# Performance work log

Hardware: AMD Instinct MI355X
Metric: run time of the kernel (lower is better)

The kernel has to match this reference:

```python
import jax, jax.numpy as jnp
import numpy as np

DIM_IN = 1024
DIM_OUT = 1024
NUM_HEADS = 16
HEAD_DIM = DIM_OUT // NUM_HEADS


def setup_inputs() -> dict:
    key = jax.random.key(0)
    ks = jax.random.split(key, 7)
    s = 1.0 / np.sqrt(DIM_IN)
    x = jax.random.normal(ks[0], (4, 2048, DIM_IN), dtype=jnp.float32)
    Wq = jax.random.uniform(ks[1], (DIM_IN, DIM_OUT), jnp.float32, -s, s)
    bq = jax.random.uniform(ks[2], (DIM_OUT,), jnp.float32, -s, s)
    Wk = jax.random.uniform(ks[3], (DIM_IN, DIM_OUT), jnp.float32, -s, s)
    bk = jax.random.uniform(ks[4], (DIM_OUT,), jnp.float32, -s, s)
    Wv = jax.random.uniform(ks[5], (DIM_IN, DIM_OUT), jnp.float32, -s, s)
    bv = jax.random.uniform(ks[6], (DIM_OUT,), jnp.float32, -s, s)
    return {"x": x, "Wq": Wq, "bq": bq, "Wk": Wk, "bk": bk, "Wv": Wv, "bv": bv}


def reference(x, Wq, bq, Wk, bk, Wv, bv):
    B, S, _ = x.shape
    scale = HEAD_DIM ** 0.5
    # project and split heads: [B, H, S, Dh]
    def heads(W, b):
        return (x @ W + b).reshape(B, S, NUM_HEADS, HEAD_DIM).transpose(0, 2, 1, 3)
    q = heads(Wq, bq)
    k = heads(Wk, bk)
    v = heads(Wv, bv)
    scores = jnp.einsum("bhqd,bhkd->bhqk", q, k) / scale  # [B,H,S,S]
    attn = jax.nn.softmax(scores, axis=-1)
    out = jnp.einsum("bhqk,bhkd->bhqd", attn, v)
    return out.transpose(0, 2, 1, 3).reshape(B, S, DIM_OUT)
```

## Files before the change

kernel.cpp:

```cpp
#include <hip/hip_runtime.h>
#include <hip/hip_bf16.h>


#define DIM  1024
#define SEQ  2048
#define BATCH 4
#define NH   16
#define HD   64

typedef __bf16 bf16x8 __attribute__((ext_vector_type(8)));
typedef short  s16x4  __attribute__((ext_vector_type(4)));
typedef float  f32x4  __attribute__((ext_vector_type(4)));
typedef unsigned int uint4v __attribute__((ext_vector_type(4)));

static __device__ __forceinline__ f32x4 mfma16(s16x4 a, s16x4 b, f32x4 c) {
    return __builtin_amdgcn_mfma_f32_16x16x16bf16_1k(a, b, c, 0, 0, 0);
}

static __device__ __forceinline__ unsigned short f2b(float f) {
    __bf16 h = (__bf16)f;
    return __builtin_bit_cast(unsigned short, h);
}

static __device__ __forceinline__ void load_lds16(const unsigned short* g,
                                                  unsigned short* l) {
    __builtin_amdgcn_global_load_lds(
        (const __attribute__((address_space(1))) void*)g,
        (__attribute__((address_space(3))) void*)l, 16, 0, 0);
}

__global__ __launch_bounds__(256) void cvt_x_k(const float* __restrict__ x,
                                               unsigned short* __restrict__ xb) {
    size_t i = ((size_t)blockIdx.x * 256 + threadIdx.x) * 8;
    const f32x4* s = (const f32x4*)(x + i);
    f32x4 a0 = s[0], a1 = s[1];
    bf16x8 v;
    for (int j = 0; j < 4; j++) { v[j] = (__bf16)a0[j]; v[4 + j] = (__bf16)a1[j]; }
    *(bf16x8*)(xb + i) = v;
}

__global__ void transpose_w_k(const float* __restrict__ Wq,
                              const float* __restrict__ Wk,
                              const float* __restrict__ Wv,
                              unsigned short* __restrict__ Wt) {
    __shared__ unsigned short t[32][33];
    int z = blockIdx.z;
    const float* W = (z == 0) ? Wq : (z == 1) ? Wk : Wv;
    unsigned short* o = Wt + (size_t)z * DIM * DIM;
    int tx = threadIdx.x;
    int n0 = blockIdx.x * 32, k0 = blockIdx.y * 32;
    for (int j = threadIdx.y; j < 32; j += 8)
        t[j][tx] = f2b(W[(size_t)(k0 + j) * DIM + n0 + tx]);
    __syncthreads();
    for (int j = threadIdx.y; j < 32; j += 8)
        o[(size_t)(n0 + j) * DIM + k0 + tx] = t[tx][j];
}

__global__ __launch_bounds__(512) void qkv_gemm_k(
    const unsigned short* __restrict__ xb,
    const unsigned short* __restrict__ WtBase,
    const float* __restrict__ bq,
    const float* __restrict__ bk,
    const float* __restrict__ bv,
    unsigned short* __restrict__ Qo,
    unsigned short* __restrict__ Ko,
    unsigned short* __restrict__ Vto) {
    __shared__ __align__(16) unsigned short As[256 * 64];
    __shared__ __align__(16) unsigned short Bs[128 * 64];
    int tid = threadIdx.x, wave = tid >> 6, lane = tid & 63;
    int quad = lane >> 4, lc = lane & 15;
    int m0 = blockIdx.y * 256, n0 = blockIdx.x * 128;
    int z = blockIdx.z;
    const unsigned short* Wt = WtBase + (size_t)z * DIM * DIM;
    int wm = (wave >> 1) * 64, wn = (wave & 1) * 64;
    int swzlo = lc & 7;

    f32x4 acc[4][4] = {};

    for (int k0 = 0; k0 < DIM; k0 += 64) {
        __syncthreads();
        #pragma unroll
        for (int p = 0; p < 4; p++) {
            int c = tid + p * 512, r = c >> 3, cc = (c & 7) ^ (r & 7);
            load_lds16(xb + (size_t)(m0 + r) * DIM + k0 + cc * 8, &As[c * 8]);
        }
        #pragma unroll
        for (int p = 0; p < 2; p++) {
            int c = tid + p * 512, r = c >> 3, cc = (c & 7) ^ (r & 7);
            load_lds16(Wt + (size_t)(n0 + r) * DIM + k0 + cc * 8, &Bs[c * 8]);
        }
        __syncthreads();
        #pragma unroll
        for (int kk = 0; kk < 2; kk++) {
            int off = ((kk * 4 + quad) ^ swzlo) * 8;
            bf16x8 af[4], bfr[4];
            for (int mt = 0; mt < 4; mt++)
                af[mt] = *(const bf16x8*)&As[(wm + mt * 16 + lc) * 64 + off];
            for (int nt = 0; nt < 4; nt++)
                bfr[nt] = *(const bf16x8*)&Bs[(wn + nt * 16 + lc) * 64 + off];
            for (int mt = 0; mt < 4; mt++)
                for (int nt = 0; nt < 4; nt++)
                    acc[mt][nt] = __builtin_amdgcn_mfma_f32_16x16x32_bf16(
                        af[mt], bfr[nt], acc[mt][nt], 0, 0, 0);
        }
    }

    const float* bias = (z == 0) ? bq : (z == 1) ? bk : bv;
    float scale = (z == 0) ? 0.18033688011112042f : 1.0f;

    if (z != 2) {
        for (int nt = 0; nt < 4; nt++) {
            int n = n0 + wn + nt * 16 + lc;
            float bvl = bias[n];
            int h = n >> 6, d = n & 63;
            for (int mt = 0; mt < 4; mt++) {
                for (int r = 0; r < 4; r++) {
                    int m = m0 + wm + mt * 16 + quad * 4 + r;
                    int b = m >> 11, s = m & 2047;
                    unsigned short ub = f2b((acc[mt][nt][r] + bvl) * scale);
                    if (z == 0)
                        Qo[((size_t)(b * NH + h) * SEQ + s) * HD + d] = ub;
                    else
                        Ko[((size_t)(b * NH + h) * SEQ + s) * HD + d] = ub;
                }
            }
        }
    } else {
        __syncthreads();
        unsigned short* T = As + wave * 1024;
        int h = (n0 + wn) >> 6;
        int d = lane;
        for (int mt = 0; mt < 4; mt++) {
            for (int nt = 0; nt < 4; nt++) {
                int n = n0 + wn + nt * 16 + lc;
                float bvl = bias[n];
                s16x4 v4;
                for (int r = 0; r < 4; r++)
                    v4[r] = (short)f2b(acc[mt][nt][r] + bvl);
                *(s16x4*)&T[(nt * 16 + lc) * 16 + quad * 4] = v4;
            }
            int s_base = m0 + wm + mt * 16;
            int b = s_base >> 11, sl = s_base & 2047;
            unsigned short* dst =
                Vto + ((size_t)(b * NH + h) * HD + d) * SEQ + sl;
            uint4v t0 = *(const uint4v*)&T[d * 16];
            uint4v t1 = *(const uint4v*)&T[d * 16 + 8];
            *(uint4v*)&dst[0] = t0;
            *(uint4v*)&dst[8] = t1;
        }
    }
}

__global__ __launch_bounds__(256) void attn_k(
    const unsigned short* __restrict__ Q,
    const unsigned short* __restrict__ K,
    const unsigned short* __restrict__ Vt,
    float* __restrict__ out) {
    __shared__ __align__(16) unsigned short KV[2 * 8192];

    int tid = threadIdx.x, wave = tid >> 6, lane = tid & 63;
    int quad = lane >> 4, lc = lane & 15;
    int swz = lc & 7;
    int bid = blockIdx.x;
    int j = bid >> 3;
    int bh = (bid & 7) * 8 + (j >> 4);
    int qt = j & 15;
    int b = bh >> 4, h = bh & 15;
    const unsigned short* Qg = Q + ((size_t)bh * SEQ + qt * 128) * HD;
    const unsigned short* Kg = K + (size_t)bh * SEQ * HD;
    const unsigned short* Vg = Vt + (size_t)bh * HD * SEQ;

    bf16x8 qf0[2], qf1[2];
    {
        const unsigned short* q0 = Qg + (size_t)(wave * 32 + lc) * HD + quad * 8;
        const unsigned short* q1 = q0 + 16 * HD;
        qf0[0] = *(const bf16x8*)q0;  qf0[1] = *(const bf16x8*)(q0 + 32);
        qf1[0] = *(const bf16x8*)q1;  qf1[1] = *(const bf16x8*)(q1 + 32);
    }

    f32x4 o[4][2] = {};
    float rsum0 = 0.0f, rsum1 = 0.0f;

    {
        unsigned short* Ks = KV;
        unsigned short* Vs = KV + 4096;
        #pragma unroll
        for (int p = 0; p < 2; p++) {
            int c = tid + p * 256, r = c >> 3, cc = c & 7;
            int sc8 = (cc ^ (r & 7)) * 8;
            load_lds16(Kg + (size_t)r * HD + sc8, &Ks[c * 8]);
            load_lds16(Vg + (size_t)r * SEQ + sc8, &Vs[c * 8]);
        }
    }

    for (int t0 = 0; t0 < SEQ; t0 += 64) {
        int cur = (t0 >> 6) & 1;
        unsigned short* Ks = KV + cur * 8192;
        unsigned short* Vs = Ks + 4096;
        __syncthreads();

        if (t0 + 64 < SEQ) {
            unsigned short* Kn = KV + (cur ^ 1) * 8192;
            unsigned short* Vn = Kn + 4096;
            #pragma unroll
            for (int p = 0; p < 2; p++) {
                int c = tid + p * 256, r = c >> 3, cc = c & 7;
                int sc8 = (cc ^ (r & 7)) * 8;
                load_lds16(Kg + (size_t)(t0 + 64 + r) * HD + sc8, &Kn[c * 8]);
                load_lds16(Vg + (size_t)r * SEQ + (t0 + 64) + sc8, &Vn[c * 8]);
            }
        }

        s16x4 pf[4][2];
        __builtin_amdgcn_s_setprio(1);
        #pragma unroll
        for (int kt = 0; kt < 4; kt++) {
            f32x4 sA = {}, sB = {};
            #pragma unroll
            for (int ks = 0; ks < 2; ks++) {
                bf16x8 kf = *(const bf16x8*)
                    &Ks[(kt * 16 + lc) * 64 + ((ks * 4 + quad) ^ swz) * 8];
                sA = __builtin_amdgcn_mfma_f32_16x16x32_bf16(kf, qf0[ks], sA, 0, 0, 0);
                sB = __builtin_amdgcn_mfma_f32_16x16x32_bf16(kf, qf1[ks], sB, 0, 0, 0);
            }
            #pragma unroll
            for (int r = 0; r < 4; r++) {
                float pa = __builtin_amdgcn_exp2f(sA[r]);
                float pb = __builtin_amdgcn_exp2f(sB[r]);
                rsum0 += pa; rsum1 += pb;
                pf[kt][0][r] = (short)f2b(pa);
                pf[kt][1][r] = (short)f2b(pb);
            }
        }

        #pragma unroll
        for (int dt = 0; dt < 4; dt++) {
            #pragma unroll
            for (int kt = 0; kt < 4; kt++) {
                s16x4 vf = *(const s16x4*)
                    &Vs[(dt * 16 + lc) * 64 +
                        ((2 * kt + (quad >> 1)) ^ swz) * 8 + (quad & 1) * 4];
                o[dt][0] = mfma16(vf, pf[kt][0], o[dt][0]);
                o[dt][1] = mfma16(vf, pf[kt][1], o[dt][1]);
            }
        }
        __builtin_amdgcn_s_setprio(0);
    }

    rsum0 += __shfl_xor(rsum0, 16); rsum0 += __shfl_xor(rsum0, 32);
    rsum1 += __shfl_xor(rsum1, 16); rsum1 += __shfl_xor(rsum1, 32);
    float inv0 = 1.0f / rsum0, inv1 = 1.0f / rsum1;

    float* o0 = out + ((size_t)b * SEQ + qt * 128 + wave * 32 + lc) * DIM
                + h * HD + quad * 4;
    float* o1 = o0 + (size_t)16 * DIM;
    #pragma unroll
    for (int dt = 0; dt < 4; dt++) {
        f32x4 s0 = o[dt][0]; s0 *= inv0;
        f32x4 s1 = o[dt][1]; s1 *= inv1;
        *(f32x4*)&o0[dt * 16] = s0;
        *(f32x4*)&o1[dt * 16] = s1;
    }
}

extern "C" void kernel_launch(void* const* d_in, const int* in_sizes, int n_in,
                              void* d_out, int out_size, void* d_ws, size_t ws_size,
                              hipStream_t stream) {
    (void)in_sizes; (void)n_in; (void)out_size; (void)ws_size;
    const float* x  = (const float*)d_in[0];
    const float* Wq = (const float*)d_in[1];
    const float* bq = (const float*)d_in[2];
    const float* Wk = (const float*)d_in[3];
    const float* bk = (const float*)d_in[4];
    const float* Wv = (const float*)d_in[5];
    const float* bv = (const float*)d_in[6];

    char* ws = (char*)d_ws;
    unsigned short* Wt = (unsigned short*)ws;
    unsigned short* Qb = (unsigned short*)(ws + (size_t)6 * 1024 * 1024);
    unsigned short* Kb = Qb + (size_t)BATCH * NH * SEQ * HD;
    unsigned short* Vb = Kb + (size_t)BATCH * NH * SEQ * HD;
    unsigned short* xb = (unsigned short*)d_out;

    cvt_x_k<<<dim3(4096), dim3(256), 0, stream>>>(x, xb);
    transpose_w_k<<<dim3(32, 32, 3), dim3(32, 8), 0, stream>>>(Wq, Wk, Wv, Wt);
    qkv_gemm_k<<<dim3(8, 32, 3), dim3(512), 0, stream>>>(xb, Wt, bq, bk, bv, Qb, Kb, Vb);
    attn_k<<<dim3(1024), dim3(256), 0, stream>>>(Qb, Kb, Vb, (float*)d_out);
}
```

Baseline: 259.0 us.

## Vectorize QKV epilogue stores and pad V tile via register-staged loads

The QKV GEMM is split into separate Q/K and V paths. For Q/K the MFMA operands are swapped so each lane holds four consecutive output columns, allowing 8-byte vector stores and a vector bias load. For V it drops the LDS transpose and writes 4-element vectors directly into the transposed layout. In attention, V tiles are staged through registers into a padded LDS layout (stride 72) instead of an XOR swizzle, with the LDS write placed between the score and PV phases. The aim is fewer scalar global stores and cheaper V fragment addressing. The cost is more register pressure, and the V prefetch now writes LDS synchronously.

```diff
diff --git a/kernel.cpp b/kernel.cpp
--- a/kernel.cpp
+++ b/kernel.cpp
@@ -73,80 +73,96 @@
     int z = blockIdx.z;
     const unsigned short* Wt = WtBase + (size_t)z * DIM * DIM;
     int wm = (wave >> 1) * 64, wn = (wave & 1) * 64;
-    int swzlo = lc & 7;
+    int swzlo = lc & 15 & 7;
 
     f32x4 acc[4][4] = {};
 
-    for (int k0 = 0; k0 < DIM; k0 += 64) {
-        __syncthreads();
-        #pragma unroll
-        for (int p = 0; p < 4; p++) {
-            int c = tid + p * 512, r = c >> 3, cc = (c & 7) ^ (r & 7);
-            load_lds16(xb + (size_t)(m0 + r) * DIM + k0 + cc * 8, &As[c * 8]);
-        }
-        #pragma unroll
-        for (int p = 0; p < 2; p++) {
-            int c = tid + p * 512, r = c >> 3, cc = (c & 7) ^ (r & 7);
-            load_lds16(Wt + (size_t)(n0 + r) * DIM + k0 + cc * 8, &Bs[c * 8]);
-        }
-        __syncthreads();
-        #pragma unroll
-        for (int kk = 0; kk < 2; kk++) {
-            int off = ((kk * 4 + quad) ^ swzlo) * 8;
-            bf16x8 af[4], bfr[4];
-            for (int mt = 0; mt < 4; mt++)
-                af[mt] = *(const bf16x8*)&As[(wm + mt * 16 + lc) * 64 + off];
-            for (int nt = 0; nt < 4; nt++)
-                bfr[nt] = *(const bf16x8*)&Bs[(wn + nt * 16 + lc) * 64 + off];
-            for (int mt = 0; mt < 4; mt++)
+    if (z != 2) {
+        for (int k0 = 0; k0 < DIM; k0 += 64) {
+            __syncthreads();
+            #pragma unroll
+            for (int p = 0; p < 4; p++) {
+                int c = tid + p * 512, r = c >> 3, cc = (c & 7) ^ (r & 7);
+                load_lds16(xb + (size_t)(m0 + r) * DIM + k0 + cc * 8, &As[c * 8]);
+            }
+            #pragma unroll
+            for (int p = 0; p < 2; p++) {
+                int c = tid + p * 512, r = c >> 3, cc = (c & 7) ^ (r & 7);
+                load_lds16(Wt + (size_t)(n0 + r) * DIM + k0 + cc * 8, &Bs[c * 8]);
+            }
+            __syncthreads();
+            #pragma unroll
+            for (int kk = 0; kk < 2; kk++) {
+                int off = ((kk * 4 + quad) ^ swzlo) * 8;
+                bf16x8 af[4], bfr[4];
+                for (int mt = 0; mt < 4; mt++)
+                    af[mt] = *(const bf16x8*)&As[(wm + mt * 16 + lc) * 64 + off];
                 for (int nt = 0; nt < 4; nt++)
-                    acc[mt][nt] = __builtin_amdgcn_mfma_f32_16x16x32_bf16(
-                        af[mt], bfr[nt], acc[mt][nt], 0, 0, 0);
-        }
-    }
-
-    const float* bias = (z == 0) ? bq : (z == 1) ? bk : bv;
-    float scale = (z == 0) ? 0.18033688011112042f : 1.0f;
-
-    if (z != 2) {
+                    bfr[nt] = *(const bf16x8*)&Bs[(wn + nt * 16 + lc) * 64 + off];
+                for (int mt = 0; mt < 4; mt++)
+                    for (int nt = 0; nt < 4; nt++)
+                        acc[mt][nt] = __builtin_amdgcn_mfma_f32_16x16x32_bf16(
+                            bfr[nt], af[mt], acc[mt][nt], 0, 0, 0);
+            }
+        }
+        const float* bias = (z == 0) ? bq : bk;
+        float scale = (z == 0) ? 0.18033688011112042f : 1.0f;
+        unsigned short* O = (z == 0) ? Qo : Ko;
+        for (int nt = 0; nt < 4; nt++) {
+            int n = n0 + wn + nt * 16 + quad * 4;
+            f32x4 bv4 = *(const f32x4*)&bias[n];
+            int h = n >> 6, d = n & 63;
+            for (int mt = 0; mt < 4; mt++) {
+                int m = m0 + wm + mt * 16 + lc;
+                int b = m >> 11, s = m & 2047;
+                s16x4 v4;
+                #pragma unroll
+                for (int r = 0; r < 4; r++)
+                    v4[r] = (short)f2b((acc[mt][nt][r] + bv4[r]) * scale);
+                *(s16x4*)&O[((size_t)(b * NH + h) * SEQ + s) * HD + d] = v4;
+            }
+        }
+    } else {
+        for (int k0 = 0; k0 < DIM; k0 += 64) {
+            __syncthreads();
+            #pragma unroll
+            for (int p = 0; p < 4; p++) {
+                int c = tid + p * 512, r = c >> 3, cc = (c & 7) ^ (r & 7);
+                load_lds16(xb + (size_t)(m0 + r) * DIM + k0 + cc * 8, &As[c * 8]);
+            }
+            #pragma unroll
+            for (int p = 0; p < 2; p++) {
+                int c = tid + p * 512, r = c >> 3, cc = (c & 7) ^ (r & 7);
+                load_lds16(Wt + (size_t)(n0 + r) * DIM + k0 + cc * 8, &Bs[c * 8]);
+            }
+            __syncthreads();
+            #pragma unroll
+            for (int kk = 0; kk < 2; kk++) {
+                int off = ((kk * 4 + quad) ^ swzlo) * 8;
+                bf16x8 af[4], bfr[4];
+                for (int mt = 0; mt < 4; mt++)
+                    af[mt] = *(const bf16x8*)&As[(wm + mt * 16 + lc) * 64 + off];
+                for (int nt = 0; nt < 4; nt++)
+                    bfr[nt] = *(const bf16x8*)&Bs[(wn + nt * 16 + lc) * 64 + off];
+                for (int mt = 0; mt < 4; mt++)
+                    for (int nt = 0; nt < 4; nt++)
+                        acc[mt][nt] = __builtin_amdgcn_mfma_f32_16x16x32_bf16(
+                            af[mt], bfr[nt], acc[mt][nt], 0, 0, 0);
+            }
+        }
         for (int nt = 0; nt < 4; nt++) {
             int n = n0 + wn + nt * 16 + lc;
-            float bvl = bias[n];
+            float bvl = bv[n];
             int h = n >> 6, d = n & 63;
             for (int mt = 0; mt < 4; mt++) {
-                for (int r = 0; r < 4; r++) {
-                    int m = m0 + wm + mt * 16 + quad * 4 + r;
-                    int b = m >> 11, s = m & 2047;
-                    unsigned short ub = f2b((acc[mt][nt][r] + bvl) * scale);
-                    if (z == 0)
-                        Qo[((size_t)(b * NH + h) * SEQ + s) * HD + d] = ub;
-                    else
-                        Ko[((size_t)(b * NH + h) * SEQ + s) * HD + d] = ub;
-                }
-            }
-        }
-    } else {
-        __syncthreads();
-        unsigned short* T = As + wave * 1024;
-        int h = (n0 + wn) >> 6;
-        int d = lane;
-        for (int mt = 0; mt < 4; mt++) {
-            for (int nt = 0; nt < 4; nt++) {
-                int n = n0 + wn + nt * 16 + lc;
-                float bvl = bias[n];
+                int m = m0 + wm + mt * 16 + quad * 4;
+                int b = m >> 11, s = m & 2047;
                 s16x4 v4;
+                #pragma unroll
                 for (int r = 0; r < 4; r++)
                     v4[r] = (short)f2b(acc[mt][nt][r] + bvl);
-                *(s16x4*)&T[(nt * 16 + lc) * 16 + quad * 4] = v4;
-            }
-            int s_base = m0 + wm + mt * 16;
-            int b = s_base >> 11, sl = s_base & 2047;
-            unsigned short* dst =
-                Vto + ((size_t)(b * NH + h) * HD + d) * SEQ + sl;
-            uint4v t0 = *(const uint4v*)&T[d * 16];
-            uint4v t1 = *(const uint4v*)&T[d * 16 + 8];
-            *(uint4v*)&dst[0] = t0;
-            *(uint4v*)&dst[8] = t1;
+                *(s16x4*)&Vto[((size_t)(b * NH + h) * HD + d) * SEQ + s] = v4;
+            }
         }
     }
 }
@@ -156,7 +172,9 @@
     const unsigned short* __restrict__ K,
     const unsigned short* __restrict__ Vt,
     float* __restrict__ out) {
-    __shared__ __align__(16) unsigned short KV[2 * 8192];
+    constexpr int LDV = 72;
+    __shared__ __align__(16) unsigned short Ksm[2 * 4096];
+    __shared__ __align__(16) unsigned short Vsm[2 * 64 * LDV];
 
     int tid = threadIdx.x, wave = tid >> 6, lane = tid & 63;
     int quad = lane >> 4, lc = lane & 15;
@@ -170,6 +188,9 @@
     const unsigned short* Kg = K + (size_t)bh * SEQ * HD;
     const unsigned short* Vg = Vt + (size_t)bh * HD * SEQ;
 
+    int sr = tid >> 3, scc = tid & 7;
+    int kcc = scc ^ (sr & 7);
+
     bf16x8 qf0[2], qf1[2];
     {
         const unsigned short* q0 = Qg + (size_t)(wave * 32 + lc) * HD + quad * 8;
@@ -182,33 +203,32 @@
     float rsum0 = 0.0f, rsum1 = 0.0f;
 
     {
-        unsigned short* Ks = KV;
-        unsigned short* Vs = KV + 4096;
-        #pragma unroll
-        for (int p = 0; p < 2; p++) {
-            int c = tid + p * 256, r = c >> 3, cc = c & 7;
-            int sc8 = (cc ^ (r & 7)) * 8;
-            load_lds16(Kg + (size_t)r * HD + sc8, &Ks[c * 8]);
-            load_lds16(Vg + (size_t)r * SEQ + sc8, &Vs[c * 8]);
-        }
+        unsigned short* Ks = Ksm;
+        unsigned short* Vs = Vsm;
+        load_lds16(Kg + (size_t)sr * HD + kcc * 8, &Ks[tid * 8]);
+        load_lds16(Kg + (size_t)(sr + 32) * HD + kcc * 8, &Ks[(tid + 256) * 8]);
+        uint4v v0 = *(const uint4v*)&Vg[(size_t)sr * SEQ + scc * 8];
+        uint4v v1 = *(const uint4v*)&Vg[(size_t)(sr + 32) * SEQ + scc * 8];
+        *(uint4v*)&Vs[sr * LDV + scc * 8] = v0;
+        *(uint4v*)&Vs[(sr + 32) * LDV + scc * 8] = v1;
     }
 
     for (int t0 = 0; t0 < SEQ; t0 += 64) {
         int cur = (t0 >> 6) & 1;
-        unsigned short* Ks = KV + cur * 8192;
-        unsigned short* Vs = Ks + 4096;
+        unsigned short* Ks = Ksm + cur * 4096;
+        unsigned short* Vs = Vsm + cur * (64 * LDV);
         __syncthreads();
 
-        if (t0 + 64 < SEQ) {
-            unsigned short* Kn = KV + (cur ^ 1) * 8192;
-            unsigned short* Vn = Kn + 4096;
-            #pragma unroll
-            for (int p = 0; p < 2; p++) {
-                int c = tid + p * 256, r = c >> 3, cc = c & 7;
-                int sc8 = (cc ^ (r & 7)) * 8;
-                load_lds16(Kg + (size_t)(t0 + 64 + r) * HD + sc8, &Kn[c * 8]);
-                load_lds16(Vg + (size_t)r * SEQ + (t0 + 64) + sc8, &Vn[c * 8]);
-            }
+        uint4v vn0, vn1;
+        bool more = (t0 + 64 < SEQ);
+        unsigned short* Kn = Ksm + (cur ^ 1) * 4096;
+        unsigned short* Vn = Vsm + (cur ^ 1) * (64 * LDV);
+        if (more) {
+            load_lds16(Kg + (size_t)(t0 + 64 + sr) * HD + kcc * 8, &Kn[tid * 8]);
+            load_lds16(Kg + (size_t)(t0 + 96 + sr) * HD + kcc * 8,
+                       &Kn[(tid + 256) * 8]);
+            vn0 = *(const uint4v*)&Vg[(size_t)sr * SEQ + t0 + 64 + scc * 8];
+            vn1 = *(const uint4v*)&Vg[(size_t)(sr + 32) * SEQ + t0 + 64 + scc * 8];
         }
 
         s16x4 pf[4][2];
@@ -232,14 +252,20 @@
                 pf[kt][1][r] = (short)f2b(pb);
             }
         }
-
+        __builtin_amdgcn_s_setprio(0);
+
+        if (more) {
+            *(uint4v*)&Vn[sr * LDV + scc * 8] = vn0;
+            *(uint4v*)&Vn[(sr + 32) * LDV + scc * 8] = vn1;
+        }
+
+        __builtin_amdgcn_s_setprio(1);
         #pragma unroll
         for (int dt = 0; dt < 4; dt++) {
             #pragma unroll
             for (int kt = 0; kt < 4; kt++) {
                 s16x4 vf = *(const s16x4*)
-                    &Vs[(dt * 16 + lc) * 64 +
-                        ((2 * kt + (quad >> 1)) ^ swz) * 8 + (quad & 1) * 4];
+                    &Vs[(dt * 16 + lc) * LDV + kt * 16 + quad * 4];
                 o[dt][0] = mfma16(vf, pf[kt][0], o[dt][0]);
                 o[dt][1] = mfma16(vf, pf[kt][1], o[dt][1]);
             }
```

Result: slower. 294.2 us (+13.6%).

## Split attention work across 8 waves with 16 query rows each

Applied to the files above, without the earlier changes.

The attention kernel goes from 4 waves each handling 32 query rows to 8 waves each handling 16 rows, and the block grows to 512 threads. K/V tile staging is now one load per thread instead of two. The aim is more waves in flight to hide latency and fewer registers per thread. The cost is that each K/V fragment read from LDS now feeds one MFMA instead of two, which doubles LDS read traffic per unit of compute.

```diff
diff --git a/kernel.cpp b/kernel.cpp
--- a/kernel.cpp
+++ b/kernel.cpp
@@ -151,7 +151,7 @@
     }
 }
 
-__global__ __launch_bounds__(256) void attn_k(
+__global__ __launch_bounds__(512) void attn_k(
     const unsigned short* __restrict__ Q,
     const unsigned short* __restrict__ K,
     const unsigned short* __restrict__ Vt,
@@ -170,27 +170,24 @@
     const unsigned short* Kg = K + (size_t)bh * SEQ * HD;
     const unsigned short* Vg = Vt + (size_t)bh * HD * SEQ;
 
-    bf16x8 qf0[2], qf1[2];
+    int sr = tid >> 3, scc = tid & 7;
+    int kcc = scc ^ (sr & 7);
+
+    bf16x8 qf[2];
     {
-        const unsigned short* q0 = Qg + (size_t)(wave * 32 + lc) * HD + quad * 8;
-        const unsigned short* q1 = q0 + 16 * HD;
-        qf0[0] = *(const bf16x8*)q0;  qf0[1] = *(const bf16x8*)(q0 + 32);
-        qf1[0] = *(const bf16x8*)q1;  qf1[1] = *(const bf16x8*)(q1 + 32);
-    }
-
-    f32x4 o[4][2] = {};
-    float rsum0 = 0.0f, rsum1 = 0.0f;
+        const unsigned short* q0 = Qg + (size_t)(wave * 16 + lc) * HD + quad * 8;
+        qf[0] = *(const bf16x8*)q0;
+        qf[1] = *(const bf16x8*)(q0 + 32);
+    }
+
+    f32x4 o[4] = {};
+    float rsum = 0.0f;
 
     {
         unsigned short* Ks = KV;
         unsigned short* Vs = KV + 4096;
-        #pragma unroll
-        for (int p = 0; p < 2; p++) {
-            int c = tid + p * 256, r = c >> 3, cc = c & 7;
-            int sc8 = (cc ^ (r & 7)) * 8;
-            load_lds16(Kg + (size_t)r * HD + sc8, &Ks[c * 8]);
-            load_lds16(Vg + (size_t)r * SEQ + sc8, &Vs[c * 8]);
-        }
+        load_lds16(Kg + (size_t)sr * HD + kcc * 8, &Ks[tid * 8]);
+        load_lds16(Vg + (size_t)sr * SEQ + kcc * 8, &Vs[tid * 8]);
     }
 
     for (int t0 = 0; t0 < SEQ; t0 += 64) {
@@ -202,34 +199,26 @@
         if (t0 + 64 < SEQ) {
             unsigned short* Kn = KV + (cur ^ 1) * 8192;
             unsigned short* Vn = Kn + 4096;
-            #pragma unroll
-            for (int p = 0; p < 2; p++) {
-                int c = tid + p * 256, r = c >> 3, cc = c & 7;
-                int sc8 = (cc ^ (r & 7)) * 8;
-                load_lds16(Kg + (size_t)(t0 + 64 + r) * HD + sc8, &Kn[c * 8]);
-                load_lds16(Vg + (size_t)r * SEQ + (t0 + 64) + sc8, &Vn[c * 8]);
-            }
-        }
-
-        s16x4 pf[4][2];
+            load_lds16(Kg + (size_t)(t0 + 64 + sr) * HD + kcc * 8, &Kn[tid * 8]);
+            load_lds16(Vg + (size_t)sr * SEQ + (t0 + 64) + kcc * 8, &Vn[tid * 8]);
+        }
+
+        s16x4 pf[4];
         __builtin_amdgcn_s_setprio(1);
         #pragma unroll
         for (int kt = 0; kt < 4; kt++) {
-            f32x4 sA = {}, sB = {};
+            f32x4 sA = {};
             #pragma unroll
             for (int ks = 0; ks < 2; ks++) {
                 bf16x8 kf = *(const bf16x8*)
                     &Ks[(kt * 16 + lc) * 64 + ((ks * 4 + quad) ^ swz) * 8];
-                sA = __builtin_amdgcn_mfma_f32_16x16x32_bf16(kf, qf0[ks], sA, 0, 0, 0);
-                sB = __builtin_amdgcn_mfma_f32_16x16x32_bf16(kf, qf1[ks], sB, 0, 0, 0);
+                sA = __builtin_amdgcn_mfma_f32_16x16x32_bf16(kf, qf[ks], sA, 0, 0, 0);
             }
             #pragma unroll
             for (int r = 0; r < 4; r++) {
                 float pa = __builtin_amdgcn_exp2f(sA[r]);
-                float pb = __builtin_amdgcn_exp2f(sB[r]);
-                rsum0 += pa; rsum1 += pb;
-                pf[kt][0][r] = (short)f2b(pa);
-                pf[kt][1][r] = (short)f2b(pb);
+                rsum += pa;
+                pf[kt][r] = (short)f2b(pa);
             }
         }
 
@@ -240,26 +229,23 @@
                 s16x4 vf = *(const s16x4*)
                     &Vs[(dt * 16 + lc) * 64 +
                         ((2 * kt + (quad >> 1)) ^ swz) * 8 + (quad & 1) * 4];
-                o[dt][0] = mfma16(vf, pf[kt][0], o[dt][0]);
-                o[dt][1] = mfma16(vf, pf[kt][1], o[dt][1]);
+                o[dt] = mfma16(vf, pf[kt], o[dt]);
             }
         }
         __builtin_amdgcn_s_setprio(0);
     }
 
-    rsum0 += __shfl_xor(rsum0, 16); rsum0 += __shfl_xor(rsum0, 32);
-    rsum1 += __shfl_xor(rsum1, 16); rsum1 += __shfl_xor(rsum1, 32);
-    float inv0 = 1.0f / rsum0, inv1 = 1.0f / rsum1;
-
-    float* o0 = out + ((size_t)b * SEQ + qt * 128 + wave * 32 + lc) * DIM
-                + h * HD + quad * 4;
-    float* o1 = o0 + (size_t)16 * DIM;
+    rsum += __shfl_xor(rsum, 16);
+    rsum += __shfl_xor(rsum, 32);
+    float inv = 1.0f / rsum;
+
+    float* orow = out + ((size_t)b * SEQ + qt * 128 + wave * 16 + lc) * DIM
+                  + h * HD + quad * 4;
     #pragma unroll
     for (int dt = 0; dt < 4; dt++) {
-        f32x4 s0 = o[dt][0]; s0 *= inv0;
-        f32x4 s1 = o[dt][1]; s1 *= inv1;
-        *(f32x4*)&o0[dt * 16] = s0;
-        *(f32x4*)&o1[dt * 16] = s1;
+        f32x4 s = o[dt];
+        s *= inv;
+        *(f32x4*)&orow[dt * 16] = s;
     }
 }
 
@@ -285,5 +271,5 @@
     cvt_x_k<<<dim3(4096), dim3(256), 0, stream>>>(x, xb);
     transpose_w_k<<<dim3(32, 32, 3), dim3(32, 8), 0, stream>>>(Wq, Wk, Wv, Wt);
     qkv_gemm_k<<<dim3(8, 32, 3), dim3(512), 0, stream>>>(xb, Wt, bq, bk, bv, Qb, Kb, Vb);
-    attn_k<<<dim3(1024), dim3(256), 0, stream>>>(Qb, Kb, Vb, (float*)d_out);
-}
+    attn_k<<<dim3(1024), dim3(512), 0, stream>>>(Qb, Kb, Vb, (float*)d_out);
+}
```

After: 268.1 us. 3.5% more time.
